# Kernel tuning notes

Measured on AMD Instinct MI355X. Metric: run time of the kernel, lower is better.

Reference implementation:

```python
import jax, jax.numpy as jnp
import numpy as np


def setup_inputs() -> dict:
    key = jax.random.key(0)
    k1, k2 = jax.random.split(key)
    B, C, H, W = 8, 256, 64, 64
    G, KS = 8, 5
    x = jax.random.normal(k1, (B, C, H, W), dtype=jnp.float32)
    w = jax.random.normal(k2, (B, G, KS * KS, H, W), dtype=jnp.float32)
    return {"x": x, "w": w}


def reference(x, w):
    # x: [B, C, H, W]; w: [B, G, ks*ks, H, W] per-pixel dynamic depthwise weights
    B, C, H, W = x.shape
    G = w.shape[1]
    K2 = w.shape[2]
    ks = int(round(K2 ** 0.5))
    pad = (ks - 1) // 2
    Cg = C // G
    xp = jnp.pad(x, ((0, 0), (0, 0), (pad, pad), (pad, pad)))
    # Extract ks*ks shifted views: [B, C, ks*ks, H, W]
    patches = jnp.stack(
        [xp[:, :, i:i + H, j:j + W] for i in range(ks) for j in range(ks)],
        axis=2,
    )
    patches = patches.reshape(B, G, Cg, K2, H, W)
    # weighted patch sum per pixel, weights shared within each channel group
    out = jnp.einsum('bgckhw,bgkhw->bgchw', patches, w)
    return out.reshape(B, C, H, W)
```

## Files before the change

kernel.cpp:

```cpp
#include <hip/hip_runtime.h>


#define B_ 8
#define C_ 256
#define G_ 8
#define CG_ 32
#define H_ 64
#define W_ 64
#define K2_ 25
#define HW_ (H_ * W_)
#define NCH 4
#define NROWS 20
#define PITCH 66
#define CHSTRIDE 1322
#define LDSW (NCH * CHSTRIDE)


#define LDW(DI, Q) (*(const float4*)(wb + (size_t)((DI) * 5 + (Q)) * HW_))

__global__ __launch_bounds__(256, 4) void ska_kernel(
    const float* __restrict__ x, const float* __restrict__ w,
    float* __restrict__ out) {
  __shared__ __align__(16) float lds[LDSW];
  const int tid = threadIdx.x;
  const int lr = tid >> 4;
  const int j = tid & 15;
  const int wcol = j * 4;

  const int blk = blockIdx.x;
  const int band = blk & 3;
  const int g = (blk >> 2) & 7;
  const int b = (blk >> 5) & 7;
  const int chunk = blk >> 8;

  const int h0 = band * 16;
  const int h = h0 + lr;

  if (tid < NCH * 42) {
    const int c = tid / 42;
    const int p = tid - c * 42;
    const int word =
        (p < 2) ? p : (2 + ((p - 2) >> 1) * PITCH + 64 + ((p - 2) & 1));
    lds[c * CHSTRIDE + word] = 0.0f;
  }

  const float* wb =
      w + (size_t)(b * G_ + g) * K2_ * HW_ + (size_t)h * W_ + wcol;
  float4 wc0 = LDW(0, 0), wc1 = LDW(0, 1), wc2 = LDW(0, 2),
         wc3 = LDW(0, 3), wc4 = LDW(0, 4);

  const size_t chan0 = (size_t)(b * C_ + g * CG_ + chunk * NCH) * HW_;
  const float* xc = x + chan0;
#pragma unroll
  for (int it = 0; it < 5; ++it) {
    const int i = tid + it * 256;
    const int c = i / 320;
    const int rem = i - c * 320;
    const int rl = rem >> 4;
    const int q = rem & 15;
    const int gr = h0 - 2 + rl;
    const bool rowok = (unsigned)gr < (unsigned)H_;
    const int grc = min(max(gr, 0), H_ - 1);
    float4 val = *(const float4*)(xc + (size_t)c * HW_ + grc * W_ + q * 4);
    if (!rowok) val = make_float4(0.f, 0.f, 0.f, 0.f);
    const int wo = c * CHSTRIDE + 2 + rl * PITCH + q * 4;
    *(float2*)&lds[wo] = make_float2(val.x, val.y);
    *(float2*)&lds[wo + 2] = make_float2(val.z, val.w);
  }

  __syncthreads();

  alignas(16) float acc[NCH][4];
#pragma unroll
  for (int c = 0; c < NCH; ++c) {
    acc[c][0] = 0.f; acc[c][1] = 0.f; acc[c][2] = 0.f; acc[c][3] = 0.f;
  }

  float4 wn0, wn1, wn2, wn3, wn4;
#pragma unroll
  for (int di = 0; di < 5; ++di) {
    if (di < 4) {
      wn0 = LDW(di + 1, 0);
      wn1 = LDW(di + 1, 1);
      wn2 = LDW(di + 1, 2);
      wn3 = LDW(di + 1, 3);
      wn4 = LDW(di + 1, 4);
    }
    const int rbase = (lr + di) * PITCH + wcol;
#pragma unroll
    for (int c = 0; c < NCH; ++c) {
      const int a0 = c * CHSTRIDE + rbase;
      alignas(16) float xr[8];
      *(float2*)&xr[0] = *(const float2*)&lds[a0];
      *(float2*)&xr[2] = *(const float2*)&lds[a0 + 2];
      *(float2*)&xr[4] = *(const float2*)&lds[a0 + 4];
      *(float2*)&xr[6] = *(const float2*)&lds[a0 + 6];
#pragma unroll
      for (int dj = 0; dj < 5; ++dj) {
        const float4 wv = (dj == 0) ? wc0
                        : (dj == 1) ? wc1
                        : (dj == 2) ? wc2
                        : (dj == 3) ? wc3
                                    : wc4;
        acc[c][0] = fmaf(xr[dj + 0], wv.x, acc[c][0]);
        acc[c][1] = fmaf(xr[dj + 1], wv.y, acc[c][1]);
        acc[c][2] = fmaf(xr[dj + 2], wv.z, acc[c][2]);
        acc[c][3] = fmaf(xr[dj + 3], wv.w, acc[c][3]);
      }
    }
    wc0 = wn0; wc1 = wn1; wc2 = wn2; wc3 = wn3; wc4 = wn4;
  }

  float* ob = out + chan0 + (size_t)h * W_ + wcol;
#pragma unroll
  for (int c = 0; c < NCH; ++c)
    *(float4*)(ob + (size_t)c * HW_) = *(const float4*)acc[c];
}

extern "C" void kernel_launch(void* const* d_in, const int* in_sizes, int n_in,
                              void* d_out, int out_size, void* d_ws,
                              size_t ws_size, hipStream_t stream) {
  const float* x = (const float*)d_in[0];
  const float* w = (const float*)d_in[1];
  float* out = (float*)d_out;
  ska_kernel<<<dim3(2048), dim3(256), 0, stream>>>(x, w, out);
}
```

Measured before the change: 111.4 us.

## Loop over channel chunks per block with weights in registers and double-buffered LDS

```diff
diff --git a/kernel.cpp b/kernel.cpp
--- a/kernel.cpp
+++ b/kernel.cpp
@@ -10,18 +10,16 @@
 #define K2_ 25
 #define HW_ (H_ * W_)
 #define NCH 4
+#define NCHUNK 8
 #define NROWS 20
 #define PITCH 66
 #define CHSTRIDE 1322
-#define LDSW (NCH * CHSTRIDE)
+#define BUFW (NCH * CHSTRIDE)
 
-
-#define LDW(DI, Q) (*(const float4*)(wb + (size_t)((DI) * 5 + (Q)) * HW_))
-
-__global__ __launch_bounds__(256, 4) void ska_kernel(
+__global__ __launch_bounds__(256, 2) void ska_kernel(
     const float* __restrict__ x, const float* __restrict__ w,
     float* __restrict__ out) {
-  __shared__ __align__(16) float lds[LDSW];
+  __shared__ __align__(16) float lds[2 * BUFW];
   const int tid = threadIdx.x;
   const int lr = tid >> 4;
   const int j = tid & 15;
@@ -30,27 +28,14 @@
   const int blk = blockIdx.x;
   const int band = blk & 3;
   const int g = (blk >> 2) & 7;
-  const int b = (blk >> 5) & 7;
-  const int chunk = blk >> 8;
+  const int b = blk >> 5;
 
   const int h0 = band * 16;
   const int h = h0 + lr;
 
-  if (tid < NCH * 42) {
-    const int c = tid / 42;
-    const int p = tid - c * 42;
-    const int word =
-        (p < 2) ? p : (2 + ((p - 2) >> 1) * PITCH + 64 + ((p - 2) & 1));
-    lds[c * CHSTRIDE + word] = 0.0f;
-  }
-
-  const float* wb =
-      w + (size_t)(b * G_ + g) * K2_ * HW_ + (size_t)h * W_ + wcol;
-  float4 wc0 = LDW(0, 0), wc1 = LDW(0, 1), wc2 = LDW(0, 2),
-         wc3 = LDW(0, 3), wc4 = LDW(0, 4);
-
-  const size_t chan0 = (size_t)(b * C_ + g * CG_ + chunk * NCH) * HW_;
-  const float* xc = x + chan0;
+  int soff[5];
+  int swo[5];
+  bool sok[5];
 #pragma unroll
   for (int it = 0; it < 5; ++it) {
     const int i = tid + it * 256;
@@ -59,62 +44,123 @@
     const int rl = rem >> 4;
     const int q = rem & 15;
     const int gr = h0 - 2 + rl;
-    const bool rowok = (unsigned)gr < (unsigned)H_;
+    sok[it] = (unsigned)gr < (unsigned)H_;
     const int grc = min(max(gr, 0), H_ - 1);
-    float4 val = *(const float4*)(xc + (size_t)c * HW_ + grc * W_ + q * 4);
-    if (!rowok) val = make_float4(0.f, 0.f, 0.f, 0.f);
-    const int wo = c * CHSTRIDE + 2 + rl * PITCH + q * 4;
-    *(float2*)&lds[wo] = make_float2(val.x, val.y);
-    *(float2*)&lds[wo + 2] = make_float2(val.z, val.w);
+    soff[it] = c * HW_ + grc * W_ + q * 4;
+    swo[it] = c * CHSTRIDE + 2 + rl * PITCH + q * 4;
   }
 
+  if (tid < NCH * 42) {
+    const int c = tid / 42;
+    const int p = tid - c * 42;
+    const int word =
+        (p < 2) ? p : (2 + ((p - 2) >> 1) * PITCH + 64 + ((p - 2) & 1));
+    lds[c * CHSTRIDE + word] = 0.0f;
+    lds[BUFW + c * CHSTRIDE + word] = 0.0f;
+  }
+
+  const size_t gbase = (size_t)(b * C_ + g * CG_) * HW_;
+  const float* xg = x + gbase;
+  float4 s0 = *(const float4*)(xg + soff[0]);
+  float4 s1 = *(const float4*)(xg + soff[1]);
+  float4 s2 = *(const float4*)(xg + soff[2]);
+  float4 s3 = *(const float4*)(xg + soff[3]);
+  float4 s4 = *(const float4*)(xg + soff[4]);
+
+  const float* wb =
+      w + (size_t)(b * G_ + g) * K2_ * HW_ + (size_t)h * W_ + wcol;
+  float4 wk[K2_];
+#pragma unroll
+  for (int k = 0; k < K2_; ++k)
+    wk[k] = *(const float4*)(wb + (size_t)k * HW_);
+
+  {
+    float4 v0 = sok[0] ? s0 : make_float4(0.f, 0.f, 0.f, 0.f);
+    float4 v1 = sok[1] ? s1 : make_float4(0.f, 0.f, 0.f, 0.f);
+    float4 v2 = sok[2] ? s2 : make_float4(0.f, 0.f, 0.f, 0.f);
+    float4 v3 = sok[3] ? s3 : make_float4(0.f, 0.f, 0.f, 0.f);
+    float4 v4 = sok[4] ? s4 : make_float4(0.f, 0.f, 0.f, 0.f);
+    *(float2*)&lds[swo[0]] = make_float2(v0.x, v0.y);
+    *(float2*)&lds[swo[0] + 2] = make_float2(v0.z, v0.w);
+    *(float2*)&lds[swo[1]] = make_float2(v1.x, v1.y);
+    *(float2*)&lds[swo[1] + 2] = make_float2(v1.z, v1.w);
+    *(float2*)&lds[swo[2]] = make_float2(v2.x, v2.y);
+    *(float2*)&lds[swo[2] + 2] = make_float2(v2.z, v2.w);
+    *(float2*)&lds[swo[3]] = make_float2(v3.x, v3.y);
+    *(float2*)&lds[swo[3] + 2] = make_float2(v3.z, v3.w);
+    *(float2*)&lds[swo[4]] = make_float2(v4.x, v4.y);
+    *(float2*)&lds[swo[4] + 2] = make_float2(v4.z, v4.w);
+  }
   __syncthreads();
 
-  alignas(16) float acc[NCH][4];
-#pragma unroll
-  for (int c = 0; c < NCH; ++c) {
-    acc[c][0] = 0.f; acc[c][1] = 0.f; acc[c][2] = 0.f; acc[c][3] = 0.f;
-  }
+  float* og = out + gbase + (size_t)h * W_ + wcol;
 
-  float4 wn0, wn1, wn2, wn3, wn4;
-#pragma unroll
-  for (int di = 0; di < 5; ++di) {
-    if (di < 4) {
-      wn0 = LDW(di + 1, 0);
-      wn1 = LDW(di + 1, 1);
-      wn2 = LDW(di + 1, 2);
-      wn3 = LDW(di + 1, 3);
-      wn4 = LDW(di + 1, 4);
+  for (int ch = 0; ch < NCHUNK; ++ch) {
+    const int p = ch & 1;
+
+    if (ch < NCHUNK - 1) {
+      const float* xn = xg + (size_t)(ch + 1) * NCH * HW_;
+      s0 = *(const float4*)(xn + soff[0]);
+      s1 = *(const float4*)(xn + soff[1]);
+      s2 = *(const float4*)(xn + soff[2]);
+      s3 = *(const float4*)(xn + soff[3]);
+      s4 = *(const float4*)(xn + soff[4]);
     }
-    const int rbase = (lr + di) * PITCH + wcol;
+
+    alignas(16) float acc[NCH][4];
 #pragma unroll
     for (int c = 0; c < NCH; ++c) {
-      const int a0 = c * CHSTRIDE + rbase;
-      alignas(16) float xr[8];
-      *(float2*)&xr[0] = *(const float2*)&lds[a0];
-      *(float2*)&xr[2] = *(const float2*)&lds[a0 + 2];
-      *(float2*)&xr[4] = *(const float2*)&lds[a0 + 4];
-      *(float2*)&xr[6] = *(const float2*)&lds[a0 + 6];
+      acc[c][0] = 0.f; acc[c][1] = 0.f; acc[c][2] = 0.f; acc[c][3] = 0.f;
+    }
+    const int pb = p * BUFW;
 #pragma unroll
-      for (int dj = 0; dj < 5; ++dj) {
-        const float4 wv = (dj == 0) ? wc0
-                        : (dj == 1) ? wc1
-                        : (dj == 2) ? wc2
-                        : (dj == 3) ? wc3
-                                    : wc4;
-        acc[c][0] = fmaf(xr[dj + 0], wv.x, acc[c][0]);
-        acc[c][1] = fmaf(xr[dj + 1], wv.y, acc[c][1]);
-        acc[c][2] = fmaf(xr[dj + 2], wv.z, acc[c][2]);
-        acc[c][3] = fmaf(xr[dj + 3], wv.w, acc[c][3]);
+    for (int di = 0; di < 5; ++di) {
+      const int rbase = pb + (lr + di) * PITCH + wcol;
+#pragma unroll
+      for (int c = 0; c < NCH; ++c) {
+        const int a0 = c * CHSTRIDE + rbase;
+        alignas(16) float xr[8];
+        *(float2*)&xr[0] = *(const float2*)&lds[a0];
+        *(float2*)&xr[2] = *(const float2*)&lds[a0 + 2];
+        *(float2*)&xr[4] = *(const float2*)&lds[a0 + 4];
+        *(float2*)&xr[6] = *(const float2*)&lds[a0 + 6];
+#pragma unroll
+        for (int dj = 0; dj < 5; ++dj) {
+          const float4 wv = wk[di * 5 + dj];
+          acc[c][0] = fmaf(xr[dj + 0], wv.x, acc[c][0]);
+          acc[c][1] = fmaf(xr[dj + 1], wv.y, acc[c][1]);
+          acc[c][2] = fmaf(xr[dj + 2], wv.z, acc[c][2]);
+          acc[c][3] = fmaf(xr[dj + 3], wv.w, acc[c][3]);
+        }
       }
     }
-    wc0 = wn0; wc1 = wn1; wc2 = wn2; wc3 = wn3; wc4 = wn4;
+
+    float* ob = og + (size_t)ch * NCH * HW_;
+    *(float4*)(ob + (size_t)0 * HW_) = *(const float4*)acc[0];
+    *(float4*)(ob + (size_t)1 * HW_) = *(const float4*)acc[1];
+    *(float4*)(ob + (size_t)2 * HW_) = *(const float4*)acc[2];
+    *(float4*)(ob + (size_t)3 * HW_) = *(const float4*)acc[3];
+
+    if (ch < NCHUNK - 1) {
+      const int ob2 = (1 - p) * BUFW;
+      float4 v0 = sok[0] ? s0 : make_float4(0.f, 0.f, 0.f, 0.f);
+      float4 v1 = sok[1] ? s1 : make_float4(0.f, 0.f, 0.f, 0.f);
+      float4 v2 = sok[2] ? s2 : make_float4(0.f, 0.f, 0.f, 0.f);
+      float4 v3 = sok[3] ? s3 : make_float4(0.f, 0.f, 0.f, 0.f);
+      float4 v4 = sok[4] ? s4 : make_float4(0.f, 0.f, 0.f, 0.f);
+      *(float2*)&lds[ob2 + swo[0]] = make_float2(v0.x, v0.y);
+      *(float2*)&lds[ob2 + swo[0] + 2] = make_float2(v0.z, v0.w);
+      *(float2*)&lds[ob2 + swo[1]] = make_float2(v1.x, v1.y);
+      *(float2*)&lds[ob2 + swo[1] + 2] = make_float2(v1.z, v1.w);
+      *(float2*)&lds[ob2 + swo[2]] = make_float2(v2.x, v2.y);
+      *(float2*)&lds[ob2 + swo[2] + 2] = make_float2(v2.z, v2.w);
+      *(float2*)&lds[ob2 + swo[3]] = make_float2(v3.x, v3.y);
+      *(float2*)&lds[ob2 + swo[3] + 2] = make_float2(v3.z, v3.w);
+      *(float2*)&lds[ob2 + swo[4]] = make_float2(v4.x, v4.y);
+      *(float2*)&lds[ob2 + swo[4] + 2] = make_float2(v4.z, v4.w);
+      __syncthreads();
+    }
   }
-
-  float* ob = out + chan0 + (size_t)h * W_ + wcol;
-#pragma unroll
-  for (int c = 0; c < NCH; ++c)
-    *(float4*)(ob + (size_t)c * HW_) = *(const float4*)acc[c];
 }
 
 extern "C" void kernel_launch(void* const* d_in, const int* in_sizes, int n_in,
@@ -123,5 +169,5 @@
   const float* x = (const float*)d_in[0];
   const float* w = (const float*)d_in[1];
   float* out = (float*)d_out;
-  ska_kernel<<<dim3(2048), dim3(256), 0, stream>>>(x, w, out);
+  ska_kernel<<<dim3(256), dim3(256), 0, stream>>>(x, w, out);
 }
```

New measurement: 111.1 us. About the same (-0.3%).

## Process four channel chunks per block with double-buffered LDS and register-cached weights

Applied to the files above, without the earlier changes.

```diff
diff --git a/kernel.cpp b/kernel.cpp
--- a/kernel.cpp
+++ b/kernel.cpp
@@ -10,18 +10,78 @@
 #define K2_ 25
 #define HW_ (H_ * W_)
 #define NCH 4
+#define NCHUNK 4
 #define NROWS 20
 #define PITCH 66
 #define CHSTRIDE 1322
-#define LDSW (NCH * CHSTRIDE)
+#define BUFW (NCH * CHSTRIDE)
 
+#define ISSUE(R0, R1, R2, R3, R4, CH)                    \
+  {                                                      \
+    const float* xn = xg + (size_t)(CH) * NCH * HW_;     \
+    R0 = *(const float4*)(xn + soff[0]);                 \
+    R1 = *(const float4*)(xn + soff[1]);                 \
+    R2 = *(const float4*)(xn + soff[2]);                 \
+    R3 = *(const float4*)(xn + soff[3]);                 \
+    R4 = *(const float4*)(xn + soff[4]);                 \
+  }
 
-#define LDW(DI, Q) (*(const float4*)(wb + (size_t)((DI) * 5 + (Q)) * HW_))
+#define STAGE(R0, R1, R2, R3, R4, PB)                                     \
+  {                                                                       \
+    const float4 z4 = make_float4(0.f, 0.f, 0.f, 0.f);                    \
+    const float4 v0 = sok[0] ? R0 : z4;                                   \
+    const float4 v1 = sok[1] ? R1 : z4;                                   \
+    const float4 v2 = sok[2] ? R2 : z4;                                   \
+    const float4 v3 = sok[3] ? R3 : z4;                                   \
+    const float4 v4 = sok[4] ? R4 : z4;                                   \
+    *(float2*)&lds[(PB) + swo[0]] = make_float2(v0.x, v0.y);              \
+    *(float2*)&lds[(PB) + swo[0] + 2] = make_float2(v0.z, v0.w);          \
+    *(float2*)&lds[(PB) + swo[1]] = make_float2(v1.x, v1.y);              \
+    *(float2*)&lds[(PB) + swo[1] + 2] = make_float2(v1.z, v1.w);          \
+    *(float2*)&lds[(PB) + swo[2]] = make_float2(v2.x, v2.y);              \
+    *(float2*)&lds[(PB) + swo[2] + 2] = make_float2(v2.z, v2.w);          \
+    *(float2*)&lds[(PB) + swo[3]] = make_float2(v3.x, v3.y);              \
+    *(float2*)&lds[(PB) + swo[3] + 2] = make_float2(v3.z, v3.w);          \
+    *(float2*)&lds[(PB) + swo[4]] = make_float2(v4.x, v4.y);              \
+    *(float2*)&lds[(PB) + swo[4] + 2] = make_float2(v4.z, v4.w);          \
+  }
 
-__global__ __launch_bounds__(256, 4) void ska_kernel(
+#define COMPUTE(PB)                                                       \
+  _Pragma("unroll") for (int c = 0; c < NCH; ++c) {                       \
+    acc[c][0] = 0.f; acc[c][1] = 0.f; acc[c][2] = 0.f; acc[c][3] = 0.f;   \
+  }                                                                       \
+  _Pragma("unroll") for (int di = 0; di < 5; ++di) {                      \
+    const int rbase = (PB) + (lr + di) * PITCH + wcol;                    \
+    _Pragma("unroll") for (int c = 0; c < NCH; ++c) {                     \
+      const int a0 = c * CHSTRIDE + rbase;                                \
+      alignas(16) float xr[8];                                            \
+      *(float2*)&xr[0] = *(const float2*)&lds[a0];                        \
+      *(float2*)&xr[2] = *(const float2*)&lds[a0 + 2];                    \
+      *(float2*)&xr[4] = *(const float2*)&lds[a0 + 4];                    \
+      *(float2*)&xr[6] = *(const float2*)&lds[a0 + 6];                    \
+      _Pragma("unroll") for (int dj = 0; dj < 5; ++dj) {                  \
+        const float4 wv = wk[di * 5 + dj];                                \
+        acc[c][0] = fmaf(xr[dj + 0], wv.x, acc[c][0]);                    \
+        acc[c][1] = fmaf(xr[dj + 1], wv.y, acc[c][1]);                    \
+        acc[c][2] = fmaf(xr[dj + 2], wv.z, acc[c][2]);                    \
+        acc[c][3] = fmaf(xr[dj + 3], wv.w, acc[c][3]);                    \
+      }                                                                   \
+    }                                                                     \
+  }
+
+#define STORE(CH)                                                         \
+  {                                                                       \
+    float* ob = og + (size_t)(CH) * NCH * HW_;                            \
+    *(float4*)(ob + (size_t)0 * HW_) = *(const float4*)acc[0];            \
+    *(float4*)(ob + (size_t)1 * HW_) = *(const float4*)acc[1];            \
+    *(float4*)(ob + (size_t)2 * HW_) = *(const float4*)acc[2];            \
+    *(float4*)(ob + (size_t)3 * HW_) = *(const float4*)acc[3];            \
+  }
+
+__global__ __launch_bounds__(256, 2) void ska_kernel(
     const float* __restrict__ x, const float* __restrict__ w,
     float* __restrict__ out) {
-  __shared__ __align__(16) float lds[LDSW];
+  __shared__ __align__(16) float lds[2 * BUFW];
   const int tid = threadIdx.x;
   const int lr = tid >> 4;
   const int j = tid & 15;
@@ -31,26 +91,14 @@
   const int band = blk & 3;
   const int g = (blk >> 2) & 7;
   const int b = (blk >> 5) & 7;
-  const int chunk = blk >> 8;
+  const int half = blk >> 8;
 
   const int h0 = band * 16;
   const int h = h0 + lr;
 
-  if (tid < NCH * 42) {
-    const int c = tid / 42;
-    const int p = tid - c * 42;
-    const int word =
-        (p < 2) ? p : (2 + ((p - 2) >> 1) * PITCH + 64 + ((p - 2) & 1));
-    lds[c * CHSTRIDE + word] = 0.0f;
-  }
-
-  const float* wb =
-      w + (size_t)(b * G_ + g) * K2_ * HW_ + (size_t)h * W_ + wcol;
-  float4 wc0 = LDW(0, 0), wc1 = LDW(0, 1), wc2 = LDW(0, 2),
-         wc3 = LDW(0, 3), wc4 = LDW(0, 4);
-
-  const size_t chan0 = (size_t)(b * C_ + g * CG_ + chunk * NCH) * HW_;
-  const float* xc = x + chan0;
+  int soff[5];
+  int swo[5];
+  bool sok[5];
 #pragma unroll
   for (int it = 0; it < 5; ++it) {
     const int i = tid + it * 256;
@@ -59,62 +107,61 @@
     const int rl = rem >> 4;
     const int q = rem & 15;
     const int gr = h0 - 2 + rl;
-    const bool rowok = (unsigned)gr < (unsigned)H_;
+    sok[it] = (unsigned)gr < (unsigned)H_;
     const int grc = min(max(gr, 0), H_ - 1);
-    float4 val = *(const float4*)(xc + (size_t)c * HW_ + grc * W_ + q * 4);
-    if (!rowok) val = make_float4(0.f, 0.f, 0.f, 0.f);
-    const int wo = c * CHSTRIDE + 2 + rl * PITCH + q * 4;
-    *(float2*)&lds[wo] = make_float2(val.x, val.y);
-    *(float2*)&lds[wo + 2] = make_float2(val.z, val.w);
+    soff[it] = c * HW_ + grc * W_ + q * 4;
+    swo[it] = c * CHSTRIDE + 2 + rl * PITCH + q * 4;
   }
 
+  if (tid < NCH * 42) {
+    const int c = tid / 42;
+    const int p = tid - c * 42;
+    const int word =
+        (p < 2) ? p : (2 + ((p - 2) >> 1) * PITCH + 64 + ((p - 2) & 1));
+    lds[c * CHSTRIDE + word] = 0.0f;
+    lds[BUFW + c * CHSTRIDE + word] = 0.0f;
+  }
+
+  const size_t chanbase = (size_t)(b * C_ + g * CG_ + half * 16) * HW_;
+  const float* xg = x + chanbase;
+  float* og = out + chanbase + (size_t)h * W_ + wcol;
+
+  float4 a0, a1, a2, a3, a4;
+  float4 b0, b1, b2, b3, b4;
+  ISSUE(a0, a1, a2, a3, a4, 0)
+  ISSUE(b0, b1, b2, b3, b4, 1)
+
+  const float* wb =
+      w + (size_t)(b * G_ + g) * K2_ * HW_ + (size_t)h * W_ + wcol;
+  float4 wk[K2_];
+#pragma unroll
+  for (int k = 0; k < K2_; ++k)
+    wk[k] = *(const float4*)(wb + (size_t)k * HW_);
+
+  STAGE(a0, a1, a2, a3, a4, 0)
   __syncthreads();
 
   alignas(16) float acc[NCH][4];
-#pragma unroll
-  for (int c = 0; c < NCH; ++c) {
-    acc[c][0] = 0.f; acc[c][1] = 0.f; acc[c][2] = 0.f; acc[c][3] = 0.f;
-  }
 
-  float4 wn0, wn1, wn2, wn3, wn4;
-#pragma unroll
-  for (int di = 0; di < 5; ++di) {
-    if (di < 4) {
-      wn0 = LDW(di + 1, 0);
-      wn1 = LDW(di + 1, 1);
-      wn2 = LDW(di + 1, 2);
-      wn3 = LDW(di + 1, 3);
-      wn4 = LDW(di + 1, 4);
-    }
-    const int rbase = (lr + di) * PITCH + wcol;
-#pragma unroll
-    for (int c = 0; c < NCH; ++c) {
-      const int a0 = c * CHSTRIDE + rbase;
-      alignas(16) float xr[8];
-      *(float2*)&xr[0] = *(const float2*)&lds[a0];
-      *(float2*)&xr[2] = *(const float2*)&lds[a0 + 2];
-      *(float2*)&xr[4] = *(const float2*)&lds[a0 + 4];
-      *(float2*)&xr[6] = *(const float2*)&lds[a0 + 6];
-#pragma unroll
-      for (int dj = 0; dj < 5; ++dj) {
-        const float4 wv = (dj == 0) ? wc0
-                        : (dj == 1) ? wc1
-                        : (dj == 2) ? wc2
-                        : (dj == 3) ? wc3
-                                    : wc4;
-        acc[c][0] = fmaf(xr[dj + 0], wv.x, acc[c][0]);
-        acc[c][1] = fmaf(xr[dj + 1], wv.y, acc[c][1]);
-        acc[c][2] = fmaf(xr[dj + 2], wv.z, acc[c][2]);
-        acc[c][3] = fmaf(xr[dj + 3], wv.w, acc[c][3]);
-      }
-    }
-    wc0 = wn0; wc1 = wn1; wc2 = wn2; wc3 = wn3; wc4 = wn4;
-  }
+  ISSUE(a0, a1, a2, a3, a4, 2)
+  COMPUTE(0)
+  STAGE(b0, b1, b2, b3, b4, BUFW)
+  __syncthreads();
+  STORE(0)
 
-  float* ob = out + chan0 + (size_t)h * W_ + wcol;
-#pragma unroll
-  for (int c = 0; c < NCH; ++c)
-    *(float4*)(ob + (size_t)c * HW_) = *(const float4*)acc[c];
+  ISSUE(b0, b1, b2, b3, b4, 3)
+  COMPUTE(BUFW)
+  STAGE(a0, a1, a2, a3, a4, 0)
+  __syncthreads();
+  STORE(1)
+
+  COMPUTE(0)
+  STAGE(b0, b1, b2, b3, b4, BUFW)
+  __syncthreads();
+  STORE(2)
+
+  COMPUTE(BUFW)
+  STORE(3)
 }
 
 extern "C" void kernel_launch(void* const* d_in, const int* in_sizes, int n_in,
@@ -123,5 +170,5 @@
   const float* x = (const float*)d_in[0];
   const float* w = (const float*)d_in[1];
   float* out = (float*)d_out;
-  ska_kernel<<<dim3(2048), dim3(256), 0, stream>>>(x, w, out);
+  ska_kernel<<<dim3(512), dim3(256), 0, stream>>>(x, w, out);
 }
```

Result: faster. 104.6 us (-6.1%).

## Keep all 25 weights in registers and stream x directly with double buffering

Applied to the files above, without the earlier changes.

```diff
diff --git a/kernel.cpp b/kernel.cpp
--- a/kernel.cpp
+++ b/kernel.cpp
@@ -9,19 +9,41 @@
 #define W_ 64
 #define K2_ 25
 #define HW_ (H_ * W_)
-#define NCH 4
-#define NROWS 20
-#define PITCH 66
-#define CHSTRIDE 1322
-#define LDSW (NCH * CHSTRIDE)
+#define NCHB 16
 
+#define LOADCH(M, L, R, XP)                                \
+  _Pragma("unroll") for (int di = 0; di < 5; ++di) {       \
+    const float* rp = (XP) + rofs[di];                     \
+    M[di] = *(const float4*)(rp + wcol);                   \
+    L[di] = *(const float2*)(rp + cl);                     \
+    R[di] = *(const float2*)(rp + cr);                     \
+  }
 
-#define LDW(DI, Q) (*(const float4*)(wb + (size_t)((DI) * 5 + (Q)) * HW_))
+#define COMPSTORE(M, L, R, OP)                             \
+  {                                                        \
+    float acc0 = 0.f, acc1 = 0.f, acc2 = 0.f, acc3 = 0.f;  \
+    _Pragma("unroll") for (int di = 0; di < 5; ++di) {     \
+      alignas(16) float xr[8];                             \
+      xr[0] = L[di].x; xr[1] = L[di].y;                    \
+      xr[2] = M[di].x; xr[3] = M[di].y;                    \
+      xr[4] = M[di].z; xr[5] = M[di].w;                    \
+      xr[6] = R[di].x; xr[7] = R[di].y;                    \
+      _Pragma("unroll") for (int dj = 0; dj < 5; ++dj) {   \
+        const float4 wv = wk[di * 5 + dj];                 \
+        acc0 = fmaf(xr[dj + 0], wv.x, acc0);               \
+        acc1 = fmaf(xr[dj + 1], wv.y, acc1);               \
+        acc2 = fmaf(xr[dj + 2], wv.z, acc2);               \
+        acc3 = fmaf(xr[dj + 3], wv.w, acc3);               \
+      }                                                    \
+    }                                                      \
+    float4 o;                                              \
+    o.x = acc0; o.y = acc1; o.z = acc2; o.w = acc3;        \
+    *(float4*)(OP) = o;                                    \
+  }
 
-__global__ __launch_bounds__(256, 4) void ska_kernel(
+__global__ __launch_bounds__(256, 2) void ska_kernel(
     const float* __restrict__ x, const float* __restrict__ w,
     float* __restrict__ out) {
-  __shared__ __align__(16) float lds[LDSW];
   const int tid = threadIdx.x;
   const int lr = tid >> 4;
   const int j = tid & 15;
@@ -31,90 +53,54 @@
   const int band = blk & 3;
   const int g = (blk >> 2) & 7;
   const int b = (blk >> 5) & 7;
-  const int chunk = blk >> 8;
+  const int half = blk >> 8;
 
   const int h0 = band * 16;
   const int h = h0 + lr;
 
-  if (tid < NCH * 42) {
-    const int c = tid / 42;
-    const int p = tid - c * 42;
-    const int word =
-        (p < 2) ? p : (2 + ((p - 2) >> 1) * PITCH + 64 + ((p - 2) & 1));
-    lds[c * CHSTRIDE + word] = 0.0f;
+  int rofs[5];
+#pragma unroll
+  for (int di = 0; di < 5; ++di) {
+    const int rr = min(max(h + di - 2, 0), H_ - 1);
+    rofs[di] = rr * W_;
   }
+  const int cl = (j == 0) ? 0 : (wcol - 2);
+  const int cr = (j == 15) ? (W_ - 4) : (wcol + 4);
+
+  const size_t chanbase = (size_t)(b * C_ + g * CG_ + half * NCHB) * HW_;
+  const float* xp = x + chanbase;
+  float* op = out + chanbase + (size_t)h * W_ + wcol;
+
+  float4 AM[5], BM[5];
+  float2 AL[5], BL[5], AR[5], BR[5];
+
+  LOADCH(AM, AL, AR, xp)
 
   const float* wb =
       w + (size_t)(b * G_ + g) * K2_ * HW_ + (size_t)h * W_ + wcol;
-  float4 wc0 = LDW(0, 0), wc1 = LDW(0, 1), wc2 = LDW(0, 2),
-         wc3 = LDW(0, 3), wc4 = LDW(0, 4);
-
-  const size_t chan0 = (size_t)(b * C_ + g * CG_ + chunk * NCH) * HW_;
-  const float* xc = x + chan0;
+  float4 wk[K2_];
 #pragma unroll
-  for (int it = 0; it < 5; ++it) {
-    const int i = tid + it * 256;
-    const int c = i / 320;
-    const int rem = i - c * 320;
-    const int rl = rem >> 4;
-    const int q = rem & 15;
-    const int gr = h0 - 2 + rl;
-    const bool rowok = (unsigned)gr < (unsigned)H_;
-    const int grc = min(max(gr, 0), H_ - 1);
-    float4 val = *(const float4*)(xc + (size_t)c * HW_ + grc * W_ + q * 4);
-    if (!rowok) val = make_float4(0.f, 0.f, 0.f, 0.f);
-    const int wo = c * CHSTRIDE + 2 + rl * PITCH + q * 4;
-    *(float2*)&lds[wo] = make_float2(val.x, val.y);
-    *(float2*)&lds[wo + 2] = make_float2(val.z, val.w);
+  for (int k = 0; k < K2_; ++k) {
+    float4 a = *(const float4*)(wb + (size_t)k * HW_);
+    const int di = k / 5, dj = k % 5;
+    const bool rok = (unsigned)(h + di - 2) < (unsigned)H_;
+    a.x = (rok && (unsigned)(wcol + 0 + dj - 2) < (unsigned)W_) ? a.x : 0.0f;
+    a.y = (rok && (unsigned)(wcol + 1 + dj - 2) < (unsigned)W_) ? a.y : 0.0f;
+    a.z = (rok && (unsigned)(wcol + 2 + dj - 2) < (unsigned)W_) ? a.z : 0.0f;
+    a.w = (rok && (unsigned)(wcol + 3 + dj - 2) < (unsigned)W_) ? a.w : 0.0f;
+    wk[k] = a;
   }
 
-  __syncthreads();
-
-  alignas(16) float acc[NCH][4];
-#pragma unroll
-  for (int c = 0; c < NCH; ++c) {
-    acc[c][0] = 0.f; acc[c][1] = 0.f; acc[c][2] = 0.f; acc[c][3] = 0.f;
+  for (int it = 0; it < NCHB / 2; ++it) {
+    LOADCH(BM, BL, BR, xp + HW_)
+    COMPSTORE(AM, AL, AR, op)
+    if (it < NCHB / 2 - 1) {
+      LOADCH(AM, AL, AR, xp + 2 * HW_)
+    }
+    COMPSTORE(BM, BL, BR, op + HW_)
+    xp += 2 * HW_;
+    op += 2 * HW_;
   }
-
-  float4 wn0, wn1, wn2, wn3, wn4;
-#pragma unroll
-  for (int di = 0; di < 5; ++di) {
-    if (di < 4) {
-      wn0 = LDW(di + 1, 0);
-      wn1 = LDW(di + 1, 1);
-      wn2 = LDW(di + 1, 2);
-      wn3 = LDW(di + 1, 3);
-      wn4 = LDW(di + 1, 4);
-    }
-    const int rbase = (lr + di) * PITCH + wcol;
-#pragma unroll
-    for (int c = 0; c < NCH; ++c) {
-      const int a0 = c * CHSTRIDE + rbase;
-      alignas(16) float xr[8];
-      *(float2*)&xr[0] = *(const float2*)&lds[a0];
-      *(float2*)&xr[2] = *(const float2*)&lds[a0 + 2];
-      *(float2*)&xr[4] = *(const float2*)&lds[a0 + 4];
-      *(float2*)&xr[6] = *(const float2*)&lds[a0 + 6];
-#pragma unroll
-      for (int dj = 0; dj < 5; ++dj) {
-        const float4 wv = (dj == 0) ? wc0
-                        : (dj == 1) ? wc1
-                        : (dj == 2) ? wc2
-                        : (dj == 3) ? wc3
-                                    : wc4;
-        acc[c][0] = fmaf(xr[dj + 0], wv.x, acc[c][0]);
-        acc[c][1] = fmaf(xr[dj + 1], wv.y, acc[c][1]);
-        acc[c][2] = fmaf(xr[dj + 2], wv.z, acc[c][2]);
-        acc[c][3] = fmaf(xr[dj + 3], wv.w, acc[c][3]);
-      }
-    }
-    wc0 = wn0; wc1 = wn1; wc2 = wn2; wc3 = wn3; wc4 = wn4;
-  }
-
-  float* ob = out + chan0 + (size_t)h * W_ + wcol;
-#pragma unroll
-  for (int c = 0; c < NCH; ++c)
-    *(float4*)(ob + (size_t)c * HW_) = *(const float4*)acc[c];
 }
 
 extern "C" void kernel_launch(void* const* d_in, const int* in_sizes, int n_in,
@@ -123,5 +109,5 @@
   const float* x = (const float*)d_in[0];
   const float* w = (const float*)d_in[1];
   float* out = (float*)d_out;
-  ska_kernel<<<dim3(2048), dim3(256), 0, stream>>>(x, w, out);
+  ska_kernel<<<dim3(512), dim3(256), 0, stream>>>(x, w, out);
 }
```

Result: slower. 125.0 us (+12.2%).
